# Optimization experiments

Hardware: AMD Instinct MI355X
Metric: run time of the kernel (lower is better)

## Reference

```python
import jax, jax.numpy as jnp
import numpy as np

B, S, H, NH = 8, 4096, 1024, 16
HD = H // NH
EPS_ATTN = 1e-6
EPS_LN = 1e-12


def setup_inputs() -> dict:
    key = jax.random.key(0)
    ks = jax.random.split(key, 10)
    s = 1.0 / np.sqrt(H)
    return {
        "input_tensor": jax.random.normal(ks[0], (B, S, H), dtype=jnp.float32),
        "attention_mask": jnp.zeros((B, S), dtype=jnp.int32),
        "Wq": jax.random.normal(ks[1], (H, H), dtype=jnp.float32) * s,
        "bq": jnp.zeros((H,), dtype=jnp.float32),
        "Wk": jax.random.normal(ks[2], (H, H), dtype=jnp.float32) * s,
        "bk": jnp.zeros((H,), dtype=jnp.float32),
        "Wv": jax.random.normal(ks[3], (H, H), dtype=jnp.float32) * s,
        "bv": jnp.zeros((H,), dtype=jnp.float32),
        "Wd": jax.random.normal(ks[4], (H, H), dtype=jnp.float32) * s,
        "bd": jnp.zeros((H,), dtype=jnp.float32),
        "gamma": jnp.ones((H,), dtype=jnp.float32),
        "beta": jnp.zeros((H,), dtype=jnp.float32),
    }


def reference(input_tensor, attention_mask, Wq, bq, Wk, bk, Wv, bv, Wd, bd, gamma, beta):
    x = input_tensor
    b, s, h = x.shape
    # QKV projections -> [B, S, NH, HD]
    q = (x @ Wq.T + bq).reshape(b, s, NH, HD)
    k = (x @ Wk.T + bk).reshape(b, s, NH, HD)
    v = (x @ Wv.T + bv).reshape(b, s, NH, HD)
    # elu+1 feature map
    q = jax.nn.elu(q) + 1.0
    k = jax.nn.elu(k) + 1.0
    # linear attention: kv state [B, NH, HD_v, HD_k]
    kv = jnp.einsum("nshd,nshm->nhmd", k, v)
    # normalizer: 1 / (q . sum_k)  -> [B, S, NH]
    z = 1.0 / jnp.einsum("nlhd,nhd->nlh", q, k.sum(axis=1) + EPS_ATTN)
    ctx = jnp.einsum("nlhd,nhmd,nlh->nlhm", q, kv, z).reshape(b, s, h)
    # output projection + residual + LayerNorm (dropout is identity in eval)
    hs = ctx @ Wd.T + bd
    hs = hs + x
    mu = hs.mean(axis=-1, keepdims=True)
    var = ((hs - mu) ** 2).mean(axis=-1, keepdims=True)
    out = (hs - mu) / jnp.sqrt(var + EPS_LN) * gamma + beta
    return out
```

## Files before the change

kernel.cpp:

```cpp
#include <hip/hip_runtime.h>
#include <cstdint>
#include <cstddef>

#define BB 8
#define SS 4096
#define HH 1024
#define NHH 16
#define HDD 64
#define MM (BB*SS)
#define KVSPLIT 16

#define BMt 256
#define BNt 256
#define BKt 64
#define NTt (HH/BKt)

typedef __attribute__((ext_vector_type(8))) short short8_t;
typedef __attribute__((ext_vector_type(4))) float f32x4;

__device__ __forceinline__ float bf2f(short u) {
  unsigned int x = ((unsigned int)(unsigned short)u) << 16;
  return __uint_as_float(x);
}
__device__ __forceinline__ short f2bf(float f) {
  unsigned int u = __float_as_uint(f);
  u += 0x7FFFu + ((u >> 16) & 1u);
  return (short)(u >> 16);
}

__device__ __forceinline__ void gload_lds16(const void* g, void* l) {
  __builtin_amdgcn_global_load_lds(
      (const __attribute__((address_space(1))) void*)g,
      (__attribute__((address_space(3))) void*)l, 16, 0, 0);
}

__global__ void cvt_bf16(const float* __restrict__ in, short* __restrict__ out, int n4) {
  int i = blockIdx.x * blockDim.x + threadIdx.x;
  if (i >= n4) return;
  float4 v = ((const float4*)in)[i];
  short4 o;
  o.x = f2bf(v.x); o.y = f2bf(v.y); o.z = f2bf(v.z); o.w = f2bf(v.w);
  ((short4*)out)[i] = o;
}

__device__ __forceinline__ void gemm256_body(
    const short* __restrict__ A, const short* __restrict__ W,
    const float* __restrict__ bias, short* __restrict__ C,
    int m0, int n0, bool act)
{
  __shared__ __align__(16) char smem[131072];

  const int tid  = threadIdx.x;
  const int lane = tid & 63;
  const int wm   = (tid >> 6) >> 2;
  const int wn   = (tid >> 6) & 3;
  const int fr   = lane & 15;
  const int fg   = lane >> 4;

  const int urow  = tid >> 3;
  const int uslot = tid & 7;
  const short* Asrc = A + (size_t)(m0 + urow) * HH + ((uslot ^ (urow & 7)) << 3);
  const short* Bsrc = W + (size_t)(n0 + urow) * HH + ((uslot ^ (urow & 7)) << 3);
  char* Adst = smem + tid * 16;
  char* Bdst = smem + 65536 + tid * 16;

#define STG8(b, kt) do { \
    gload_lds16(Asrc + (size_t)(0*64) * HH + (kt) * 64, Adst + (b) * 32768 + 0*8192); \
    gload_lds16(Asrc + (size_t)(1*64) * HH + (kt) * 64, Adst + (b) * 32768 + 1*8192); \
    gload_lds16(Asrc + (size_t)(2*64) * HH + (kt) * 64, Adst + (b) * 32768 + 2*8192); \
    gload_lds16(Asrc + (size_t)(3*64) * HH + (kt) * 64, Adst + (b) * 32768 + 3*8192); \
    gload_lds16(Bsrc + (size_t)(0*64) * HH + (kt) * 64, Bdst + (b) * 32768 + 0*8192); \
    gload_lds16(Bsrc + (size_t)(1*64) * HH + (kt) * 64, Bdst + (b) * 32768 + 1*8192); \
    gload_lds16(Bsrc + (size_t)(2*64) * HH + (kt) * 64, Bdst + (b) * 32768 + 2*8192); \
    gload_lds16(Bsrc + (size_t)(3*64) * HH + (kt) * 64, Bdst + (b) * 32768 + 3*8192); \
  } while (0)

  const char* pA = smem + (wm * 128 + fr) * 128;
  const char* pB = smem + 65536 + (wn * 64 + fr) * 128;
  const int sw0 = ((fg)     ^ (fr & 7)) << 4;
  const int sw1 = ((4 + fg) ^ (fr & 7)) << 4;

  f32x4 acc[8][4] = {};
  short8_t bfrag[2][4];

  STG8(0, 0);
  asm volatile("s_waitcnt vmcnt(0)" ::: "memory");
  __builtin_amdgcn_s_barrier();
  __builtin_amdgcn_sched_barrier(0);

  #pragma unroll 2
  for (int kt = 0; kt < NTt; ++kt) {
    const int buf = kt & 1;
    const int ao = buf * 32768;
    short8_t af[4];

    #pragma unroll
    for (int j = 0; j < 4; j++) bfrag[0][j] = *(const short8_t*)(pB + ao + j * 2048 + sw0);
    #pragma unroll
    for (int i = 0; i < 4; i++) af[i] = *(const short8_t*)(pA + ao + i * 2048 + sw0);
    if (kt + 1 < NTt) STG8(buf ^ 1, kt + 1);
    __builtin_amdgcn_s_barrier();
    __builtin_amdgcn_sched_barrier(0);
    __builtin_amdgcn_s_setprio(1);
    #pragma unroll
    for (int i = 0; i < 4; i++)
      #pragma unroll
      for (int j = 0; j < 4; j++)
        acc[i][j] = __builtin_amdgcn_mfma_f32_16x16x32_bf16(af[i], bfrag[0][j], acc[i][j], 0, 0, 0);
    __builtin_amdgcn_s_setprio(0);
    __builtin_amdgcn_s_barrier();
    __builtin_amdgcn_sched_barrier(0);

    #pragma unroll
    for (int j = 0; j < 4; j++) bfrag[1][j] = *(const short8_t*)(pB + ao + j * 2048 + sw1);
    #pragma unroll
    for (int i = 0; i < 4; i++) af[i] = *(const short8_t*)(pA + ao + i * 2048 + sw1);
    __builtin_amdgcn_s_barrier();
    __builtin_amdgcn_sched_barrier(0);
    __builtin_amdgcn_s_setprio(1);
    #pragma unroll
    for (int i = 0; i < 4; i++)
      #pragma unroll
      for (int j = 0; j < 4; j++)
        acc[i][j] = __builtin_amdgcn_mfma_f32_16x16x32_bf16(af[i], bfrag[1][j], acc[i][j], 0, 0, 0);
    __builtin_amdgcn_s_setprio(0);
    __builtin_amdgcn_s_barrier();
    __builtin_amdgcn_sched_barrier(0);

    #pragma unroll
    for (int i = 0; i < 4; i++) af[i] = *(const short8_t*)(pA + ao + 8192 + i * 2048 + sw0);
    __builtin_amdgcn_s_barrier();
    __builtin_amdgcn_sched_barrier(0);
    __builtin_amdgcn_s_setprio(1);
    #pragma unroll
    for (int i = 0; i < 4; i++)
      #pragma unroll
      for (int j = 0; j < 4; j++)
        acc[4 + i][j] = __builtin_amdgcn_mfma_f32_16x16x32_bf16(af[i], bfrag[0][j], acc[4 + i][j], 0, 0, 0);
    __builtin_amdgcn_s_setprio(0);
    __builtin_amdgcn_s_barrier();
    __builtin_amdgcn_sched_barrier(0);

    #pragma unroll
    for (int i = 0; i < 4; i++) af[i] = *(const short8_t*)(pA + ao + 8192 + i * 2048 + sw1);
    __builtin_amdgcn_s_barrier();
    __builtin_amdgcn_sched_barrier(0);
    __builtin_amdgcn_s_setprio(1);
    #pragma unroll
    for (int i = 0; i < 4; i++)
      #pragma unroll
      for (int j = 0; j < 4; j++)
        acc[4 + i][j] = __builtin_amdgcn_mfma_f32_16x16x32_bf16(af[i], bfrag[1][j], acc[4 + i][j], 0, 0, 0);
    __builtin_amdgcn_s_setprio(0);
    asm volatile("s_waitcnt vmcnt(0)" ::: "memory");
    __builtin_amdgcn_s_barrier();
    __builtin_amdgcn_sched_barrier(0);
  }
#undef STG8

  short* sC = (short*)smem;
  float bvj[4];
  #pragma unroll
  for (int j = 0; j < 4; j++) bvj[j] = bias[n0 + wn * 64 + j * 16 + fr];

  #pragma unroll
  for (int h = 0; h < 2; ++h) {
    if (wm == h) {
      #pragma unroll
      for (int ii = 0; ii < 8; ii++) {
        const int rel = (ii >> 2) * 64 + (ii & 3) * 16 + fg * 4;
        #pragma unroll
        for (int j = 0; j < 4; j++) {
          const int col = wn * 64 + j * 16 + fr;
          #pragma unroll
          for (int r = 0; r < 4; r++) {
            float v = acc[ii][j][r] + bvj[j];
            if (act) v = (v > 0.f) ? (v + 1.f) : __expf(v);
            sC[(rel + r) * 264 + col] = f2bf(v);
          }
        }
      }
    }
    __syncthreads();
    const int crow = tid >> 5;
    const int cch  = (tid & 31) * 8;
    #pragma unroll
    for (int p = 0; p < 8; p++) {
      const int row = p * 16 + crow;
      *(short8_t*)(C + (size_t)(m0 + h * 128 + row) * HH + n0 + cch) =
          *(const short8_t*)(sC + row * 264 + cch);
    }
    __syncthreads();
  }
}

__global__ __launch_bounds__(512, 2) void qkv_gemm(
    const short* __restrict__ xb,
    const short* __restrict__ Wqb, const short* __restrict__ Wkb, const short* __restrict__ Wvb,
    const float* __restrict__ bq, const float* __restrict__ bk, const float* __restrict__ bv,
    short* __restrict__ Qo, short* __restrict__ Ko, short* __restrict__ Vo)
{
  const int which = blockIdx.x >> 2;
  const int n0 = (blockIdx.x & 3) * BNt;
  const int m0 = blockIdx.y * BMt;
  const short* W  = (which == 0) ? Wqb : (which == 1) ? Wkb : Wvb;
  const float* bs = (which == 0) ? bq  : (which == 1) ? bk  : bv;
  short* C        = (which == 0) ? Qo  : (which == 1) ? Ko  : Vo;
  gemm256_body(xb, W, bs, C, m0, n0, which < 2);
}

__global__ __launch_bounds__(512, 2) void dproj_gemm(
    const short* __restrict__ A, const short* __restrict__ W,
    const float* __restrict__ bias, short* __restrict__ C)
{
  gemm256_body(A, W, bias, C, blockIdx.y * BMt, blockIdx.x * BNt, false);
}

__global__ __launch_bounds__(256) void kv_part_kernel(
    const short* __restrict__ K_, const short* __restrict__ V_,
    float* __restrict__ kvpart, float* __restrict__ kspart)
{
  __shared__ __align__(16) float sK[32 * 64];
  __shared__ __align__(16) float sV[32 * 64];
  const int h = blockIdx.x, b = blockIdx.y, sp = blockIdx.z;
  const int t = threadIdx.x;
  const int m = t & 63;
  const int dg = (t >> 6) * 16;
  const int lrow = t >> 3;
  const int lcol = (t & 7) * 8;
  const int SC = SS / KVSPLIT;
  float acc[16] = {};
  float ks = 0.f;
  const size_t base = ((size_t)b * SS + (size_t)sp * SC) * HH + (size_t)h * HDD;
  const short* Kp = K_ + base + (size_t)lrow * HH + lcol;
  const short* Vp = V_ + base + (size_t)lrow * HH + lcol;

  for (int sc = 0; sc < SC; sc += 32) {
    short8_t k8 = *(const short8_t*)(Kp + (size_t)sc * HH);
    short8_t v8 = *(const short8_t*)(Vp + (size_t)sc * HH);
    __syncthreads();
    #pragma unroll
    for (int j = 0; j < 8; j++) {
      sK[lrow * 64 + lcol + j] = bf2f(k8[j]);
      sV[lrow * 64 + lcol + j] = bf2f(v8[j]);
    }
    __syncthreads();
    if (t < 64) {
      #pragma unroll
      for (int ss = 0; ss < 32; ss++) ks += sK[ss * 64 + t];
    }
    #pragma unroll 4
    for (int ss = 0; ss < 32; ss++) {
      const float vm = sV[ss * 64 + m];
      const float* kr = sK + ss * 64 + dg;
      #pragma unroll
      for (int j = 0; j < 16; j++) acc[j] += kr[j] * vm;
    }
  }

  const int bh = b * NHH + h;
  float* kvp = kvpart + (size_t)(bh * KVSPLIT + sp) * 4096 + m * 64 + dg;
  #pragma unroll
  for (int j = 0; j < 16; j += 4) {
    f32x4 o;
    o[0] = acc[j]; o[1] = acc[j+1]; o[2] = acc[j+2]; o[3] = acc[j+3];
    *(f32x4*)(kvp + j) = o;
  }
  if (t < 64) kspart[(bh * KVSPLIT + sp) * 64 + t] = ks;
}

__global__ __launch_bounds__(256) void kv_reduce_kernel(
    const float* __restrict__ kvpart, const float* __restrict__ kspart,
    short* __restrict__ kvbf, float* __restrict__ ksum)
{
  const int bh = blockIdx.x;
  const int t = threadIdx.x;
  const float* src = kvpart + (size_t)bh * KVSPLIT * 4096;
  #pragma unroll
  for (int i = 0; i < 4; i++) {
    const int idx = t + i * 256;
    f32x4 s = {};
    #pragma unroll 4
    for (int p = 0; p < KVSPLIT; p++)
      s += ((const f32x4*)(src + (size_t)p * 4096))[idx];
    short4 o;
    o.x = f2bf(s[0]); o.y = f2bf(s[1]); o.z = f2bf(s[2]); o.w = f2bf(s[3]);
    ((short4*)(kvbf + (size_t)bh * 4096))[idx] = o;
  }
  if (t < 64) {
    float s = 0.f;
    #pragma unroll
    for (int p = 0; p < KVSPLIT; p++) s += kspart[(bh * KVSPLIT + p) * 64 + t];
    ksum[bh * 64 + t] = s + 1e-6f;
  }
}

__global__ __launch_bounds__(256) void ctx_mfma(
    const short* __restrict__ Q, const short* __restrict__ kvbf,
    const float* __restrict__ ksum, short* __restrict__ ctx)
{
  __shared__ __align__(16) short sB[64 * 72];
  __shared__ float sks[64];
  __shared__ float sz[256];
  const int b = blockIdx.z, h = blockIdx.y;
  const int t = threadIdx.x;
  const int lane = t & 63, wave = t >> 6;
  const int s0 = blockIdx.x * 256;
  const int bh = b * NHH + h;

  {
    const short8_t* src = (const short8_t*)(kvbf + (size_t)bh * 4096);
    const int m = t >> 2, c = (t & 3) * 16;
    short8_t v0 = src[t * 2], v1 = src[t * 2 + 1];
    *(short8_t*)(sB + m * 72 + c)     = v0;
    *(short8_t*)(sB + m * 72 + c + 8) = v1;
  }
  if (t < 64) sks[t] = ksum[bh * 64 + t];
  __syncthreads();

  {
    const short* qp = Q + (size_t)(b * SS + s0 + t) * HH + h * HDD;
    float zden = 0.f;
    #pragma unroll
    for (int i = 0; i < 8; i++) {
      short8_t q8 = *(const short8_t*)(qp + i * 8);
      #pragma unroll
      for (int j = 0; j < 8; j++) zden += bf2f(q8[j]) * sks[i * 8 + j];
    }
    sz[t] = 1.f / zden;
  }
  __syncthreads();

  const int fr = lane & 15, fk = (lane >> 4) * 8;
  const int wrow = wave * 64;
  f32x4 acc[4][4] = {};
  const short* qbase = Q + (size_t)(b * SS + s0 + wrow + fr) * HH + h * HDD + fk;
  #pragma unroll
  for (int k0 = 0; k0 < 64; k0 += 32) {
    short8_t af[4], wf[4];
    #pragma unroll
    for (int i = 0; i < 4; i++)
      af[i] = *(const short8_t*)(qbase + (size_t)(i * 16) * HH + k0);
    #pragma unroll
    for (int j = 0; j < 4; j++)
      wf[j] = *(const short8_t*)(sB + (j * 16 + fr) * 72 + fk + k0);
    #pragma unroll
    for (int i = 0; i < 4; i++) {
      #pragma unroll
      for (int j = 0; j < 4; j++) {
        acc[i][j] = __builtin_amdgcn_mfma_f32_16x16x32_bf16(af[i], wf[j], acc[i][j], 0, 0, 0);
      }
    }
  }

  const int cr = (lane >> 4) * 4, cc = lane & 15;
  short* cp = ctx + ((size_t)(b * SS + s0)) * HH + h * HDD;
  #pragma unroll
  for (int j = 0; j < 4; j++) {
    const int col = j * 16 + cc;
    #pragma unroll
    for (int i = 0; i < 4; i++) {
      #pragma unroll
      for (int r = 0; r < 4; r++) {
        const int row = wrow + i * 16 + cr + r;
        cp[(size_t)row * HH + col] = f2bf(acc[i][j][r] * sz[row]);
      }
    }
  }
}

__global__ __launch_bounds__(256) void ln_kernel(
    const short* __restrict__ P, const float* __restrict__ x,
    const float* __restrict__ gamma, const float* __restrict__ beta,
    float* __restrict__ out)
{
  const int row = blockIdx.x;
  const int t = threadIdx.x;
  const short* pr = P + (size_t)row * HH;
  const float* xr = x + (size_t)row * HH;
  short4 p4 = ((const short4*)pr)[t];
  float4 x4 = ((const float4*)xr)[t];
  float h0 = bf2f(p4.x) + x4.x;
  float h1 = bf2f(p4.y) + x4.y;
  float h2 = bf2f(p4.z) + x4.z;
  float h3 = bf2f(p4.w) + x4.w;
  float s1 = h0 + h1 + h2 + h3;
  float s2 = h0*h0 + h1*h1 + h2*h2 + h3*h3;
  #pragma unroll
  for (int o = 32; o > 0; o >>= 1) {
    s1 += __shfl_xor(s1, o);
    s2 += __shfl_xor(s2, o);
  }
  __shared__ float red[8];
  const int wv = t >> 6, ln = t & 63;
  if (ln == 0) { red[wv] = s1; red[4 + wv] = s2; }
  __syncthreads();
  const float S1 = red[0] + red[1] + red[2] + red[3];
  const float S2 = red[4] + red[5] + red[6] + red[7];
  const float mu  = S1 * (1.f / HH);
  const float var = S2 * (1.f / HH) - mu * mu;
  const float inv = rsqrtf(var + 1e-12f);
  float4 g4 = ((const float4*)gamma)[t];
  float4 b4 = ((const float4*)beta)[t];
  float4 o4;
  o4.x = (h0 - mu) * inv * g4.x + b4.x;
  o4.y = (h1 - mu) * inv * g4.y + b4.y;
  o4.z = (h2 - mu) * inv * g4.z + b4.z;
  o4.w = (h3 - mu) * inv * g4.w + b4.w;
  ((float4*)(out + (size_t)row * HH))[t] = o4;
}

extern "C" void kernel_launch(void* const* d_in, const int* in_sizes, int n_in,
                              void* d_out, int out_size, void* d_ws, size_t ws_size,
                              hipStream_t stream)
{
  const float* x     = (const float*)d_in[0];
  const float* Wq    = (const float*)d_in[2];
  const float* bq    = (const float*)d_in[3];
  const float* Wk    = (const float*)d_in[4];
  const float* bk    = (const float*)d_in[5];
  const float* Wv    = (const float*)d_in[6];
  const float* bv    = (const float*)d_in[7];
  const float* Wd    = (const float*)d_in[8];
  const float* bd    = (const float*)d_in[9];
  const float* gamma = (const float*)d_in[10];
  const float* beta  = (const float*)d_in[11];
  float* out = (float*)d_out;

  char* ws = (char*)d_ws;
  const size_t MB64 = 67108864;
  short* xb  = (short*)(ws + 0 * MB64);
  short* Qb  = (short*)(ws + 1 * MB64);
  short* Kb  = (short*)(ws + 2 * MB64);
  short* Vb  = (short*)(ws + 3 * MB64);
  short* Cb  = (short*)(ws + 4 * MB64);
  short* Wqb = (short*)(ws + 5 * MB64 + 0 * 2097152);
  short* Wkb = (short*)(ws + 5 * MB64 + 1 * 2097152);
  short* Wvb = (short*)(ws + 5 * MB64 + 2 * 2097152);
  short* Wdb = (short*)(ws + 5 * MB64 + 3 * 2097152);
  short* kvbf= (short*)(ws + 5 * MB64 + 4 * 2097152);
  float* ksb = (float*)(ws + 5 * MB64 + 5 * 2097152);
  float* kvpart = (float*)(ws + 4 * MB64);
  float* kspart = kvpart + (size_t)128 * KVSPLIT * 4096;
  short* Pb  = Qb;

  cvt_bf16<<<(MM * HH / 4) / 256, 256, 0, stream>>>(x,  xb,  MM * HH / 4);
  cvt_bf16<<<(HH * HH / 4) / 256, 256, 0, stream>>>(Wq, Wqb, HH * HH / 4);
  cvt_bf16<<<(HH * HH / 4) / 256, 256, 0, stream>>>(Wk, Wkb, HH * HH / 4);
  cvt_bf16<<<(HH * HH / 4) / 256, 256, 0, stream>>>(Wv, Wvb, HH * HH / 4);
  cvt_bf16<<<(HH * HH / 4) / 256, 256, 0, stream>>>(Wd, Wdb, HH * HH / 4);

  qkv_gemm<<<dim3(12, MM / BMt), 512, 0, stream>>>(xb, Wqb, Wkb, Wvb, bq, bk, bv, Qb, Kb, Vb);

  kv_part_kernel<<<dim3(NHH, BB, KVSPLIT), 256, 0, stream>>>(Kb, Vb, kvpart, kspart);
  kv_reduce_kernel<<<BB * NHH, 256, 0, stream>>>(kvpart, kspart, kvbf, ksb);
  ctx_mfma<<<dim3(SS / 256, NHH, BB), 256, 0, stream>>>(Qb, kvbf, ksb, Cb);

  dproj_gemm<<<dim3(HH / BNt, MM / BMt), 512, 0, stream>>>(Cb, Wdb, bd, Pb);
  ln_kernel<<<MM, 256, 0, stream>>>(Pb, x, gamma, beta, out);
}
```

Baseline: 753.7 us.

## Interleave A/B half-tile loads with staged waits and remap warp rows

The GEMM stops issuing all eight global-to-LDS loads for the next K tile at once. It splits them into A and B half-tile groups spread across the four MFMA phases and prefetches part of tile kt+2 into the current buffer once the rows it needs have been consumed. Full vmcnt(0) waits become vmcnt(8) partial waits, so loads stay in flight across iterations. The A-row ownership of warps is remapped so each warp group reads interleaved 64-row blocks, and the epilogue is rewritten to match. This adds fragile ordering that depends on exact vmcnt counting and buffer reuse.

```diff
diff --git a/kernel.cpp b/kernel.cpp
--- a/kernel.cpp
+++ b/kernel.cpp
@@ -52,7 +52,7 @@
 
   const int tid  = threadIdx.x;
   const int lane = tid & 63;
-  const int wm   = (tid >> 6) >> 2;
+  const int wm2  = (tid >> 6) >> 2;
   const int wn   = (tid >> 6) & 3;
   const int fr   = lane & 15;
   const int fg   = lane >> 4;
@@ -64,27 +64,32 @@
   char* Adst = smem + tid * 16;
   char* Bdst = smem + 65536 + tid * 16;
 
-#define STG8(b, kt) do { \
-    gload_lds16(Asrc + (size_t)(0*64) * HH + (kt) * 64, Adst + (b) * 32768 + 0*8192); \
-    gload_lds16(Asrc + (size_t)(1*64) * HH + (kt) * 64, Adst + (b) * 32768 + 1*8192); \
-    gload_lds16(Asrc + (size_t)(2*64) * HH + (kt) * 64, Adst + (b) * 32768 + 2*8192); \
-    gload_lds16(Asrc + (size_t)(3*64) * HH + (kt) * 64, Adst + (b) * 32768 + 3*8192); \
-    gload_lds16(Bsrc + (size_t)(0*64) * HH + (kt) * 64, Bdst + (b) * 32768 + 0*8192); \
-    gload_lds16(Bsrc + (size_t)(1*64) * HH + (kt) * 64, Bdst + (b) * 32768 + 1*8192); \
-    gload_lds16(Bsrc + (size_t)(2*64) * HH + (kt) * 64, Bdst + (b) * 32768 + 2*8192); \
-    gload_lds16(Bsrc + (size_t)(3*64) * HH + (kt) * 64, Bdst + (b) * 32768 + 3*8192); \
+#define STG_AH(b, kt, h) do { \
+    gload_lds16(Asrc + (size_t)((h)*2+0) * 64 * HH + (kt) * 64, Adst + (b) * 32768 + ((h)*2+0) * 8192); \
+    gload_lds16(Asrc + (size_t)((h)*2+1) * 64 * HH + (kt) * 64, Adst + (b) * 32768 + ((h)*2+1) * 8192); \
   } while (0)
-
-  const char* pA = smem + (wm * 128 + fr) * 128;
+#define STG_BH(b, kt, h) do { \
+    gload_lds16(Bsrc + (size_t)((h)*2+0) * 64 * HH + (kt) * 64, Bdst + (b) * 32768 + ((h)*2+0) * 8192); \
+    gload_lds16(Bsrc + (size_t)((h)*2+1) * 64 * HH + (kt) * 64, Bdst + (b) * 32768 + ((h)*2+1) * 8192); \
+  } while (0)
+
+  const char* pA = smem + fr * 128;
   const char* pB = smem + 65536 + (wn * 64 + fr) * 128;
   const int sw0 = ((fg)     ^ (fr & 7)) << 4;
   const int sw1 = ((4 + fg) ^ (fr & 7)) << 4;
+  const int rowA = wm2 * 8192;
 
   f32x4 acc[8][4] = {};
   short8_t bfrag[2][4];
 
-  STG8(0, 0);
-  asm volatile("s_waitcnt vmcnt(0)" ::: "memory");
+  STG_AH(0, 0, 0);
+  STG_BH(0, 0, 0);
+  STG_BH(0, 0, 1);
+  STG_AH(0, 0, 1);
+  STG_AH(1, 1, 0);
+  STG_BH(1, 1, 0);
+  STG_BH(1, 1, 1);
+  asm volatile("s_waitcnt vmcnt(8)" ::: "memory");
   __builtin_amdgcn_s_barrier();
   __builtin_amdgcn_sched_barrier(0);
 
@@ -97,8 +102,8 @@
     #pragma unroll
     for (int j = 0; j < 4; j++) bfrag[0][j] = *(const short8_t*)(pB + ao + j * 2048 + sw0);
     #pragma unroll
-    for (int i = 0; i < 4; i++) af[i] = *(const short8_t*)(pA + ao + i * 2048 + sw0);
-    if (kt + 1 < NTt) STG8(buf ^ 1, kt + 1);
+    for (int i = 0; i < 4; i++) af[i] = *(const short8_t*)(pA + ao + rowA + i * 2048 + sw0);
+    if (kt + 1 < NTt) STG_AH(buf ^ 1, kt + 1, 1);
     __builtin_amdgcn_s_barrier();
     __builtin_amdgcn_sched_barrier(0);
     __builtin_amdgcn_s_setprio(1);
@@ -114,7 +119,7 @@
     #pragma unroll
     for (int j = 0; j < 4; j++) bfrag[1][j] = *(const short8_t*)(pB + ao + j * 2048 + sw1);
     #pragma unroll
-    for (int i = 0; i < 4; i++) af[i] = *(const short8_t*)(pA + ao + i * 2048 + sw1);
+    for (int i = 0; i < 4; i++) af[i] = *(const short8_t*)(pA + ao + rowA + i * 2048 + sw1);
     __builtin_amdgcn_s_barrier();
     __builtin_amdgcn_sched_barrier(0);
     __builtin_amdgcn_s_setprio(1);
@@ -124,11 +129,14 @@
       for (int j = 0; j < 4; j++)
         acc[i][j] = __builtin_amdgcn_mfma_f32_16x16x32_bf16(af[i], bfrag[1][j], acc[i][j], 0, 0, 0);
     __builtin_amdgcn_s_setprio(0);
-    __builtin_amdgcn_s_barrier();
-    __builtin_amdgcn_sched_barrier(0);
-
-    #pragma unroll
-    for (int i = 0; i < 4; i++) af[i] = *(const short8_t*)(pA + ao + 8192 + i * 2048 + sw0);
+    if (kt < NTt - 2) asm volatile("s_waitcnt vmcnt(8)" ::: "memory");
+    else              asm volatile("s_waitcnt vmcnt(0)" ::: "memory");
+    __builtin_amdgcn_s_barrier();
+    __builtin_amdgcn_sched_barrier(0);
+
+    #pragma unroll
+    for (int i = 0; i < 4; i++) af[i] = *(const short8_t*)(pA + ao + 16384 + rowA + i * 2048 + sw0);
+    if (kt + 2 < NTt) { STG_AH(buf, kt + 2, 0); STG_BH(buf, kt + 2, 0); }
     __builtin_amdgcn_s_barrier();
     __builtin_amdgcn_sched_barrier(0);
     __builtin_amdgcn_s_setprio(1);
@@ -142,7 +150,8 @@
     __builtin_amdgcn_sched_barrier(0);
 
     #pragma unroll
-    for (int i = 0; i < 4; i++) af[i] = *(const short8_t*)(pA + ao + 8192 + i * 2048 + sw1);
+    for (int i = 0; i < 4; i++) af[i] = *(const short8_t*)(pA + ao + 16384 + rowA + i * 2048 + sw1);
+    if (kt + 2 < NTt) STG_BH(buf, kt + 2, 1);
     __builtin_amdgcn_s_barrier();
     __builtin_amdgcn_sched_barrier(0);
     __builtin_amdgcn_s_setprio(1);
@@ -152,11 +161,13 @@
       for (int j = 0; j < 4; j++)
         acc[4 + i][j] = __builtin_amdgcn_mfma_f32_16x16x32_bf16(af[i], bfrag[1][j], acc[4 + i][j], 0, 0, 0);
     __builtin_amdgcn_s_setprio(0);
-    asm volatile("s_waitcnt vmcnt(0)" ::: "memory");
-    __builtin_amdgcn_s_barrier();
-    __builtin_amdgcn_sched_barrier(0);
-  }
-#undef STG8
+    if (kt < NTt - 2) asm volatile("s_waitcnt vmcnt(8)" ::: "memory");
+    else              asm volatile("s_waitcnt vmcnt(0)" ::: "memory");
+    __builtin_amdgcn_s_barrier();
+    __builtin_amdgcn_sched_barrier(0);
+  }
+#undef STG_AH
+#undef STG_BH
 
   short* sC = (short*)smem;
   float bvj[4];
@@ -165,19 +176,16 @@
 
   #pragma unroll
   for (int h = 0; h < 2; ++h) {
-    if (wm == h) {
-      #pragma unroll
-      for (int ii = 0; ii < 8; ii++) {
-        const int rel = (ii >> 2) * 64 + (ii & 3) * 16 + fg * 4;
+    #pragma unroll
+    for (int i = 0; i < 4; i++) {
+      #pragma unroll
+      for (int j = 0; j < 4; j++) {
+        const int col = wn * 64 + j * 16 + fr;
         #pragma unroll
-        for (int j = 0; j < 4; j++) {
-          const int col = wn * 64 + j * 16 + fr;
-          #pragma unroll
-          for (int r = 0; r < 4; r++) {
-            float v = acc[ii][j][r] + bvj[j];
-            if (act) v = (v > 0.f) ? (v + 1.f) : __expf(v);
-            sC[(rel + r) * 264 + col] = f2bf(v);
-          }
+        for (int r = 0; r < 4; r++) {
+          float v = acc[h * 4 + i][j][r] + bvj[j];
+          if (act) v = (v > 0.f) ? (v + 1.f) : __expf(v);
+          sC[(wm2 * 64 + i * 16 + fg * 4 + r) * 264 + col] = f2bf(v);
         }
       }
     }
```

After: 721.2 us. 4.3% less time.
